# Optimization experiments

Hardware: AMD Instinct MI355X
Metric: run time of the kernel (lower is better)

The kernel has to match this reference:

```python
import jax, jax.numpy as jnp
import numpy as np


def setup_inputs() -> dict:
    key = jax.random.key(0)
    B, D, C, H = 4096, 64, 128, 512
    ks = jax.random.split(key, 6)
    return {
        "q_z_x_params": jax.random.normal(ks[0], (B, C), jnp.float32),
        "eps": jax.random.normal(ks[1], (B, D), jnp.float32),
        "W1": jax.random.normal(ks[2], (D + C, H), jnp.float32) / np.sqrt(D + C).astype(np.float32),
        "b1": jnp.zeros((H,), jnp.float32),
        "W2": jax.random.normal(ks[3], (H, H), jnp.float32) / np.sqrt(H).astype(np.float32),
        "b2": jnp.zeros((H,), jnp.float32),
        "W3": jax.random.normal(ks[4], (H, 2 * D), jnp.float32) / np.sqrt(H).astype(np.float32),
        "b3": jnp.zeros((2 * D,), jnp.float32),
    }


def _made_masks(D, C, H):
    # Standard MADE degrees, natural ordering; context columns fully connected.
    m_in = np.arange(1, D + 1)                      # input degrees 1..D
    m_h = (np.arange(H) % (D - 1)) + 1              # hidden degrees 1..D-1
    M1 = np.concatenate([m_h[None, :] >= m_in[:, None],
                         np.ones((C, H), bool)], axis=0)   # (D+C, H)
    M2 = m_h[None, :] >= m_h[:, None]               # (H, H)
    m_out = np.tile(np.arange(1, D + 1), 2)         # (2D,) mean||prescale
    M3 = m_out[None, :] > m_h[:, None]              # (H, 2D)
    f32 = jnp.float32
    return jnp.asarray(M1, f32), jnp.asarray(M2, f32), jnp.asarray(M3, f32)


def reference(q_z_x_params, eps, W1, b1, W2, b2, W3, b3):
    B, D = eps.shape
    C = q_z_x_params.shape[1]
    H = W2.shape[0]
    M1, M2, M3 = _made_masks(D, C, H)
    mW1, mW2, mW3 = W1 * M1, W2 * M2, W3 * M3

    def made(z):
        x = jnp.concatenate([z, q_z_x_params], axis=1)   # (B, D+C)
        h1 = jax.nn.relu(x @ mW1 + b1)
        h2 = jax.nn.relu(h1 @ mW2 + b2)
        out = h2 @ mW3 + b3                              # (B, 2D)
        return out[:, :D], out[:, D:]

    def step(z, i):
        mean, prescale = made(z)
        mu_i = jnp.take(mean, i, axis=1)                 # (B,)
        scale_i = jax.nn.softplus(jnp.take(prescale, i, axis=1))
        z_i = mu_i + scale_i * jnp.take(eps, i, axis=1)  # reparameterized Normal sample
        z = z.at[:, i].set(z_i)
        return z, None

    z0 = jnp.zeros((B, D), eps.dtype)
    z_sample, _ = jax.lax.scan(step, z0, jnp.arange(D))
    return z_sample
```

## Files before the change

kernel.cpp:

```cpp
#include <hip/hip_runtime.h>
#include <math.h>

#define DD 64
#define CC 128
#define HH 512
#define BATCH 4096

typedef __attribute__((ext_vector_type(2))) float f32x2;
typedef unsigned long long u64;

__device__ __forceinline__ f32x2 splat2(float x) { f32x2 v; v[0] = x; v[1] = x; return v; }

__device__ __forceinline__ f32x2 pk_fma_s(u64 hpair, f32x2 b, f32x2 c) {
    f32x2 d;
    asm("v_pk_fma_f32 %0, %1, %2, %3" : "=v"(d) : "s"(hpair), "v"(b), "v"(c));
    return d;
}

__device__ __forceinline__ float fast_softplus(float x) {
    float t = exp2f(-fabsf(x) * 1.44269504f);
    return fmaxf(x, 0.f) + 0.69314718f * log2f(1.f + t);
}

__device__ __forceinline__ float bcast(float x, int l) {
    return __int_as_float(__builtin_amdgcn_readlane(__float_as_int(x), l));
}
__device__ __forceinline__ u64 rl_pair(float x, int l) {
    unsigned u = (unsigned)__builtin_amdgcn_readlane(__float_as_int(x), l);
    return ((u64)u << 32) | u;
}

typedef const __attribute__((address_space(1))) void* as1_cptr;
typedef __attribute__((address_space(3))) void* as3_ptr;
__device__ __forceinline__ void glds16(const float* g, float* l) {
    __builtin_amdgcn_global_load_lds((as1_cptr)g, (as3_ptr)l, 16, 0, 0);
}

__global__ __launch_bounds__(512, 4) void made_sample(
    const float* __restrict__ ctx,
    const float* __restrict__ eps,
    const float* __restrict__ W1,
    const float* __restrict__ b1,
    const float* __restrict__ W2,
    const float* __restrict__ b2,
    const float* __restrict__ W3,
    const float* __restrict__ b3,
    float* __restrict__ out)
{
    const int lane  = threadIdx.x & 63;
    const int w     = threadIdx.x >> 6;
    const int rrow  = blockIdx.x * 8 + w;
    const int jbase = 8 * lane;

    __shared__ float sbuf[2][10 * HH];
    __shared__ float w3sb[2][5 * 256];

    int deg[8];
    #pragma unroll
    for (int u = 0; u < 8; ++u) deg[u] = (jbase + u) % 63 + 1;

    auto load8v = [&](const float* base_, f32x2* r_) {
        float4 a = *(const float4*)(base_ + lane * 4);
        float4 b = *(const float4*)(base_ + 256 + lane * 4);
        r_[0][0] = a.x; r_[0][1] = a.y; r_[1][0] = a.z; r_[1][1] = a.w;
        r_[2][0] = b.x; r_[2][1] = b.y; r_[3][0] = b.z; r_[3][1] = b.w;
    };
    auto stage_row = [&](const float* src, float* dst) {
        glds16(src + lane * 8,     dst);
        glds16(src + lane * 8 + 4, dst + 256);
    };
    auto stage_w3pair = [&](int k0, int k1, float* dst) {
        const float* g = (lane < 32) ? (W3 + k0 * (2 * DD) + lane * 4)
                                     : (W3 + k1 * (2 * DD) + (lane - 32) * 4);
        glds16(g, dst);
    };

    f32x2 p1[4], p2[4], acc;
    #pragma unroll
    for (int j = 0; j < 4; ++j) {
        p1[j][0] = b1[jbase + 2 * j]; p1[j][1] = b1[jbase + 2 * j + 1];
        p2[j][0] = b2[jbase + 2 * j]; p2[j][1] = b2[jbase + 2 * j + 1];
    }
    acc = splat2(0.f);

    const float ca = ctx[rrow * CC + lane];
    const float cb = ctx[rrow * CC + 64 + lane];
    const float ep = eps[rrow * DD + lane];
    const float b3m = b3[lane];
    const float b3p = b3[64 + lane];

    auto stage_ctx = [&](int ch, float* buf) {
        stage_row(W1 + (DD + 8 * ch + w) * HH, buf + w * HH);
    };
    auto stage_step = [&](int in, float* buf, float* w3buf) {
        if (in == 0) {
            if (w == 1) stage_row(W1, buf + 9 * HH);
            return;
        }
        const int basen = in - 1;
        const bool h9n = basen < 8;
        stage_row(W2 + (basen + 63 * w) * HH, buf + w * HH);
        if (w == 0 && h9n) stage_row(W2 + (basen + 504) * HH, buf + 8 * HH);
        if (w == 1) stage_row(W1 + in * HH, buf + 9 * HH);
        if (w >= 2 && w <= 5) {
            const int p = w - 2;
            stage_w3pair(basen + 63 * (2 * p), basen + 63 * (2 * p + 1),
                         w3buf + p * 256);
        }
        if (w == 6 && h9n)
            stage_w3pair(basen + 504, basen + 504, w3buf + 4 * 256);
    };

    stage_ctx(0, sbuf[0]);
    __syncthreads();
    #pragma unroll 1
    for (int ch = 0; ch < 16; ++ch) {
        float* cur = sbuf[ch & 1];
        if (ch < 15) stage_ctx(ch + 1, sbuf[(ch + 1) & 1]);
        else         stage_step(0, sbuf[0], w3sb[0]);
        #pragma unroll
        for (int q = 0; q < 8; ++q) {
            f32x2 cw[4];
            load8v(cur + q * HH, cw);
            const int c = 8 * ch + q;
            const u64 cvp = rl_pair((ch < 8) ? ca : cb, c & 63);
            #pragma unroll
            for (int j = 0; j < 4; ++j) p1[j] = pk_fma_s(cvp, cw[j], p1[j]);
        }
        __syncthreads();
    }

    float z = 0.f;

    #pragma unroll 1
    for (int i = 0; i < DD; ++i) {
        float* cur = sbuf[i & 1];
        const float* w3s = w3sb[i & 1];

        if (i < 63) stage_step(i + 1, sbuf[(i + 1) & 1], w3sb[(i + 1) & 1]);

        f32x2 w1v[4];
        load8v(cur + 9 * HH, w1v);

        if (i > 0) {
            const int base = i - 1;
            const bool h9 = base < 8;

            float m0 = 0.f;
            #pragma unroll
            for (int u = 0; u < 8; ++u)
                m0 = (deg[u] == i) ? p1[u >> 1][u & 1] : m0;
            m0 = fmaxf(m0, 0.f);

            #pragma unroll
            for (int t = 0; t < 8; ++t) {
                const int k = base + 63 * t;
                f32x2 wv[4];
                load8v(cur + t * HH, wv);
                const u64 h0 = rl_pair(m0, k >> 3);
                #pragma unroll
                for (int j = 0; j < 4; ++j) p2[j] = pk_fma_s(h0, wv[j], p2[j]);
            }
            if (h9) {
                f32x2 wv[4];
                load8v(cur + 8 * HH, wv);
                const u64 h0 = rl_pair(m0, 63);
                #pragma unroll
                for (int j = 0; j < 4; ++j) p2[j] = pk_fma_s(h0, wv[j], p2[j]);
            }

            float g0 = 0.f;
            #pragma unroll
            for (int u = 0; u < 8; ++u)
                g0 = (deg[u] == i) ? p2[u >> 1][u & 1] : g0;
            g0 = fmaxf(g0, 0.f);

            #pragma unroll
            for (int t = 0; t < 8; ++t) {
                const int k = base + 63 * t;
                const float wa = w3s[t * 128 + lane];
                const float wb = w3s[t * 128 + 64 + lane];
                const float h0 = bcast(g0, k >> 3);
                acc[0] = fmaf(h0, wa, acc[0]);
                acc[1] = fmaf(h0, wb, acc[1]);
            }
            if (h9) {
                const float wa = w3s[8 * 128 + lane];
                const float wb = w3s[8 * 128 + 64 + lane];
                const float h0 = bcast(g0, 63);
                acc[0] = fmaf(h0, wa, acc[0]);
                acc[1] = fmaf(h0, wb, acc[1]);
            }
        }

        {
            const float am = acc[0] + b3m;
            const float ap = acc[1] + b3p;
            const float sp = fast_softplus(ap);
            const float zc = fmaf(sp, ep, am);
            if (lane == i) z = bcast(zc, i);
            const u64 zp = rl_pair(zc, i);
            #pragma unroll
            for (int j = 0; j < 4; ++j) p1[j] = pk_fma_s(zp, w1v[j], p1[j]);
        }

        __syncthreads();
    }

    out[rrow * DD + lane] = z;
}

extern "C" void kernel_launch(void* const* d_in, const int* in_sizes, int n_in,
                              void* d_out, int out_size, void* d_ws, size_t ws_size,
                              hipStream_t stream) {
    const float* ctx = (const float*)d_in[0];
    const float* eps = (const float*)d_in[1];
    const float* W1  = (const float*)d_in[2];
    const float* b1  = (const float*)d_in[3];
    const float* W2  = (const float*)d_in[4];
    const float* b2  = (const float*)d_in[5];
    const float* W3  = (const float*)d_in[6];
    const float* b3  = (const float*)d_in[7];
    (void)d_ws; (void)ws_size; (void)in_sizes; (void)n_in; (void)out_size;

    made_sample<<<BATCH / 8, 512, 0, stream>>>(ctx, eps, W1, b1, W2, b2, W3, b3,
                                               (float*)d_out);
}
```

Measured before the change: 175.0 us.

## Store W1/W2 as bf16 in workspace and stage halved rows into LDS

Adds a pre-pass kernel that rounds W1 and W2 to bf16 in the workspace, and the main kernel stages these half-size rows into LDS and widens them to fp32 before the packed FMAs. This halves global-to-LDS traffic and LDS footprint per step, which may allow more resident blocks and less memory stall. It costs an extra kernel launch and conversion pass each call, plus reduced weight precision that could perturb the sequential sampling output.

```diff
diff --git a/kernel.cpp b/kernel.cpp
--- a/kernel.cpp
+++ b/kernel.cpp
@@ -8,6 +8,7 @@
 
 typedef __attribute__((ext_vector_type(2))) float f32x2;
 typedef unsigned long long u64;
+typedef unsigned short u16;
 
 __device__ __forceinline__ f32x2 splat2(float x) { f32x2 v; v[0] = x; v[1] = x; return v; }
 
@@ -32,16 +33,28 @@
 
 typedef const __attribute__((address_space(1))) void* as1_cptr;
 typedef __attribute__((address_space(3))) void* as3_ptr;
-__device__ __forceinline__ void glds16(const float* g, float* l) {
+__device__ __forceinline__ void glds16(const void* g, void* l) {
     __builtin_amdgcn_global_load_lds((as1_cptr)g, (as3_ptr)l, 16, 0, 0);
+}
+
+__global__ void cvt_w(const float* __restrict__ W1, const float* __restrict__ W2,
+                      u16* __restrict__ o) {
+    const int n1 = (DD + CC) * HH;
+    const int n  = n1 + HH * HH;
+    for (int i = blockIdx.x * blockDim.x + threadIdx.x; i < n;
+         i += gridDim.x * blockDim.x) {
+        const float x = (i < n1) ? W1[i] : W2[i - n1];
+        const unsigned u = __float_as_uint(x);
+        o[i] = (u16)((u + 0x7fffu + ((u >> 16) & 1u)) >> 16);
+    }
 }
 
 __global__ __launch_bounds__(512, 4) void made_sample(
     const float* __restrict__ ctx,
     const float* __restrict__ eps,
-    const float* __restrict__ W1,
+    const u16*   __restrict__ w1b,
     const float* __restrict__ b1,
-    const float* __restrict__ W2,
+    const u16*   __restrict__ w2b,
     const float* __restrict__ b2,
     const float* __restrict__ W3,
     const float* __restrict__ b3,
@@ -52,22 +65,26 @@
     const int rrow  = blockIdx.x * 8 + w;
     const int jbase = 8 * lane;
 
-    __shared__ float sbuf[2][10 * HH];
+    __shared__ u16   sbuf[2][10 * HH];
     __shared__ float w3sb[2][5 * 256];
 
     int deg[8];
     #pragma unroll
     for (int u = 0; u < 8; ++u) deg[u] = (jbase + u) % 63 + 1;
 
-    auto load8v = [&](const float* base_, f32x2* r_) {
-        float4 a = *(const float4*)(base_ + lane * 4);
-        float4 b = *(const float4*)(base_ + 256 + lane * 4);
-        r_[0][0] = a.x; r_[0][1] = a.y; r_[1][0] = a.z; r_[1][1] = a.w;
-        r_[2][0] = b.x; r_[2][1] = b.y; r_[3][0] = b.z; r_[3][1] = b.w;
-    };
-    auto stage_row = [&](const float* src, float* dst) {
-        glds16(src + lane * 8,     dst);
-        glds16(src + lane * 8 + 4, dst + 256);
+    auto load8bf = [&](const u16* base_, f32x2* w_) {
+        const uint4 v = *(const uint4*)(base_ + lane * 8);
+        w_[0][0] = __uint_as_float(v.x << 16);
+        w_[0][1] = __uint_as_float(v.x & 0xFFFF0000u);
+        w_[1][0] = __uint_as_float(v.y << 16);
+        w_[1][1] = __uint_as_float(v.y & 0xFFFF0000u);
+        w_[2][0] = __uint_as_float(v.z << 16);
+        w_[2][1] = __uint_as_float(v.z & 0xFFFF0000u);
+        w_[3][0] = __uint_as_float(v.w << 16);
+        w_[3][1] = __uint_as_float(v.w & 0xFFFF0000u);
+    };
+    auto stage_row = [&](const u16* src, u16* dst) {
+        glds16(src + lane * 8, dst);
     };
     auto stage_w3pair = [&](int k0, int k1, float* dst) {
         const float* g = (lane < 32) ? (W3 + k0 * (2 * DD) + lane * 4)
@@ -89,19 +106,19 @@
     const float b3m = b3[lane];
     const float b3p = b3[64 + lane];
 
-    auto stage_ctx = [&](int ch, float* buf) {
-        stage_row(W1 + (DD + 8 * ch + w) * HH, buf + w * HH);
-    };
-    auto stage_step = [&](int in, float* buf, float* w3buf) {
+    auto stage_ctx = [&](int ch, u16* buf) {
+        stage_row(w1b + (DD + 8 * ch + w) * HH, buf + w * HH);
+    };
+    auto stage_step = [&](int in, u16* buf, float* w3buf) {
         if (in == 0) {
-            if (w == 1) stage_row(W1, buf + 9 * HH);
+            if (w == 1) stage_row(w1b, buf + 9 * HH);
             return;
         }
         const int basen = in - 1;
         const bool h9n = basen < 8;
-        stage_row(W2 + (basen + 63 * w) * HH, buf + w * HH);
-        if (w == 0 && h9n) stage_row(W2 + (basen + 504) * HH, buf + 8 * HH);
-        if (w == 1) stage_row(W1 + in * HH, buf + 9 * HH);
+        stage_row(w2b + (basen + 63 * w) * HH, buf + w * HH);
+        if (w == 0 && h9n) stage_row(w2b + (basen + 504) * HH, buf + 8 * HH);
+        if (w == 1) stage_row(w1b + in * HH, buf + 9 * HH);
         if (w >= 2 && w <= 5) {
             const int p = w - 2;
             stage_w3pair(basen + 63 * (2 * p), basen + 63 * (2 * p + 1),
@@ -115,13 +132,13 @@
     __syncthreads();
     #pragma unroll 1
     for (int ch = 0; ch < 16; ++ch) {
-        float* cur = sbuf[ch & 1];
+        u16* cur = sbuf[ch & 1];
         if (ch < 15) stage_ctx(ch + 1, sbuf[(ch + 1) & 1]);
         else         stage_step(0, sbuf[0], w3sb[0]);
         #pragma unroll
         for (int q = 0; q < 8; ++q) {
             f32x2 cw[4];
-            load8v(cur + q * HH, cw);
+            load8bf(cur + q * HH, cw);
             const int c = 8 * ch + q;
             const u64 cvp = rl_pair((ch < 8) ? ca : cb, c & 63);
             #pragma unroll
@@ -134,13 +151,13 @@
 
     #pragma unroll 1
     for (int i = 0; i < DD; ++i) {
-        float* cur = sbuf[i & 1];
+        u16* cur = sbuf[i & 1];
         const float* w3s = w3sb[i & 1];
 
         if (i < 63) stage_step(i + 1, sbuf[(i + 1) & 1], w3sb[(i + 1) & 1]);
 
         f32x2 w1v[4];
-        load8v(cur + 9 * HH, w1v);
+        load8bf(cur + 9 * HH, w1v);
 
         if (i > 0) {
             const int base = i - 1;
@@ -156,14 +173,14 @@
             for (int t = 0; t < 8; ++t) {
                 const int k = base + 63 * t;
                 f32x2 wv[4];
-                load8v(cur + t * HH, wv);
+                load8bf(cur + t * HH, wv);
                 const u64 h0 = rl_pair(m0, k >> 3);
                 #pragma unroll
                 for (int j = 0; j < 4; ++j) p2[j] = pk_fma_s(h0, wv[j], p2[j]);
             }
             if (h9) {
                 f32x2 wv[4];
-                load8v(cur + 8 * HH, wv);
+                load8bf(cur + 8 * HH, wv);
                 const u64 h0 = rl_pair(m0, 63);
                 #pragma unroll
                 for (int j = 0; j < 4; ++j) p2[j] = pk_fma_s(h0, wv[j], p2[j]);
@@ -223,6 +240,10 @@
     const float* b3  = (const float*)d_in[7];
     (void)d_ws; (void)ws_size; (void)in_sizes; (void)n_in; (void)out_size;
 
-    made_sample<<<BATCH / 8, 512, 0, stream>>>(ctx, eps, W1, b1, W2, b2, W3, b3,
-                                               (float*)d_out);
-}
+    u16* wsb = (u16*)d_ws;
+    cvt_w<<<704, 512, 0, stream>>>(W1, W2, wsb);
+    made_sample<<<BATCH / 8, 512, 0, stream>>>(ctx, eps,
+                                               wsb, b1,
+                                               wsb + (DD + CC) * HH, b2,
+                                               W3, b3, (float*)d_out);
+}
```

After: 207.5 us. +18.6%, slower.
